# Optimization experiments

Hardware: AMD Instinct MI355X
Metric: run time of the kernel (lower is better)

## Reference

```python
import jax, jax.numpy as jnp
import numpy as np

D, H, DH, FF = 768, 12, 64, 3072

def setup_inputs() -> dict:
    key = jax.random.key(0)
    ks = iter(jax.random.split(key, 40))
    B, Li, Lt = 128, 197, 64
    nrm = lambda shape, s=0.02: (jax.random.normal(next(ks), shape, jnp.float32) * s)
    inp = {}
    inp['image_feats'] = jax.random.normal(next(ks), (B, Li, D), jnp.float32)
    inp['image_att_score'] = jax.random.uniform(next(ks), (B, Li), jnp.float32)
    inp['text_feats'] = jax.random.normal(next(ks), (B, Lt, D), jnp.float32)
    inp['text_att_score'] = jax.random.uniform(next(ks), (B, Lt), jnp.float32)
    inp['tokens'] = jax.random.randint(next(ks), (B, Lt), 0, 1000)
    # BatchNorm1d bottlenecks (inference: running stats)
    for p in ('img', 'txt'):
        inp[f'bn_{p}_g'] = jnp.ones((D,), jnp.float32)
        inp[f'bn_{p}_b'] = jnp.zeros((D,), jnp.float32)
        inp[f'bn_{p}_m'] = nrm((D,), 0.1)
        inp[f'bn_{p}_v'] = jax.random.uniform(next(ks), (D,), jnp.float32, 0.5, 1.5)
    # ResidualAttention (1 layer, cross): ln1, ln2, qkv/out proj, mlp 768->3072->768
    inp['ln1_g'] = jnp.ones((D,), jnp.float32); inp['ln1_b'] = jnp.zeros((D,), jnp.float32)
    inp['ln2_g'] = jnp.ones((D,), jnp.float32); inp['ln2_b'] = jnp.zeros((D,), jnp.float32)
    for n in ('Wq', 'Wk', 'Wv', 'Wo'):
        inp[n] = nrm((D, D))
    for n in ('bq', 'bk', 'bv', 'bo'):
        inp[n] = jnp.zeros((D,), jnp.float32)
    inp['W1'] = nrm((D, FF)); inp['b1'] = jnp.zeros((FF,), jnp.float32)
    inp['W2'] = nrm((FF, D)); inp['b2'] = jnp.zeros((D,), jnp.float32)
    inp['img_K'] = 59   # int(197 * 0.3)
    inp['text_K'] = 19  # int(64 * 0.3)
    return inp

def _ln(x, g, b):
    mu = jnp.mean(x, -1, keepdims=True)
    v = jnp.mean((x - mu) ** 2, -1, keepdims=True)
    return (x - mu) * jax.lax.rsqrt(v + 1e-5) * g + b

def _bn(x, g, b, m, v):
    return (x - m) * jax.lax.rsqrt(v + 1e-5) * g + b

def _cross_block(x, y, key_mask, ln1_g, ln1_b, ln2_g, ln2_b,
                 Wq, bq, Wk, bk, Wv, bv, Wo, bo, W1, b1, W2, b2):
    # cross-attn: queries from x, keys/values from y; pre-LN residual block
    B, Lq, _ = x.shape
    Lk = y.shape[1]
    qn = _ln(x, ln1_g, ln1_b)
    kn = _ln(y, ln1_g, ln1_b)
    q = (qn @ Wq + bq).reshape(B, Lq, H, DH)
    k = (kn @ Wk + bk).reshape(B, Lk, H, DH)
    v = (kn @ Wv + bv).reshape(B, Lk, H, DH)
    scores = jnp.einsum('bqhd,bkhd->bhqk', q, k) / np.float32(np.sqrt(DH))
    if key_mask is not None:  # True = padding -> masked out
        scores = jnp.where(key_mask[:, None, None, :], jnp.float32(-1e9), scores)
    a = jax.nn.softmax(scores, axis=-1)
    att = jnp.einsum('bhqk,bkhd->bqhd', a, v).reshape(B, Lq, D) @ Wo + bo
    x = x + att
    h = _ln(x, ln2_g, ln2_b)
    x = x + jax.nn.gelu(h @ W1 + b1, approximate=False) @ W2 + b2
    return x

def _select(feats, score, K):
    # zero CLS score, full descending sort via top_k, gather token subsets
    L = score.shape[1]
    score = score * jnp.concatenate([jnp.zeros_like(score[:, :1]), jnp.ones_like(score[:, 1:])], axis=1)
    _, idx = jax.lax.top_k(score, L)  # [B, L] sorted desc
    cls = feats[:, :1, :]
    sel1 = jnp.take_along_axis(feats, idx[:, :K, None], axis=1)
    sel2 = jnp.take_along_axis(feats, idx[:, K:2 * K, None], axis=1)
    return jnp.concatenate([cls, sel1], 1), jnp.concatenate([cls, sel2], 1)

def reference(image_feats, image_att_score, text_feats, text_att_score, tokens,
              bn_img_g, bn_img_b, bn_img_m, bn_img_v,
              bn_txt_g, bn_txt_b, bn_txt_m, bn_txt_v,
              ln1_g, ln1_b, ln2_g, ln2_b,
              Wq, bq, Wk, bk, Wv, bv, Wo, bo, W1, b1, W2, b2,
              img_K, text_K):
    blk = lambda x, y, m: _cross_block(x, y, m, ln1_g, ln1_b, ln2_g, ln2_b,
                                       Wq, bq, Wk, bk, Wv, bv, Wo, bo, W1, b1, W2, b2)
    img_global = _bn(image_feats[:, 0, :], bn_img_g, bn_img_b, bn_img_m, bn_img_v)
    text_global = _bn(text_feats[:, 0, :], bn_txt_g, bn_txt_b, bn_txt_m, bn_txt_v)
    text_masks = (tokens == 0)  # True where padding
    img_sel1, img_sel2 = _select(image_feats, image_att_score, img_K)
    image_part1 = blk(img_sel1, image_feats, None)
    image_part2 = blk(img_sel2, image_feats, None)
    txt_sel1, txt_sel2 = _select(text_feats, text_att_score, text_K)
    text_part1 = blk(txt_sel1, text_feats, text_masks)
    text_part2 = blk(txt_sel2, text_feats, text_masks)
    return (img_global, text_global, image_part1, image_part2, text_part1, text_part2)
```

## Files before the change

### kernel.cpp

```cpp
#include <hip/hip_runtime.h>

typedef unsigned short u16;
typedef __bf16 bf16x8 __attribute__((ext_vector_type(8)));
typedef float f32x4 __attribute__((ext_vector_type(4)));

__device__ __forceinline__ float b2f(u16 u) { return __builtin_bit_cast(float, (unsigned)u << 16); }
__device__ __forceinline__ u16 f2b(float f) {
  unsigned x = __builtin_bit_cast(unsigned, f);
  x += 0x7fffu + ((x >> 16) & 1u);
  return (u16)(x >> 16);
}

__device__ __forceinline__ void gload16(const u16* g, u16* l) {
  auto gp = (__attribute__((address_space(1))) void*)(void*)const_cast<u16*>(g);
  auto lp = (__attribute__((address_space(3))) void*)(void*)l;
  __builtin_amdgcn_global_load_lds(gp, lp, 16, 0, 0);
}

__device__ __forceinline__ f32x4 mfma16(bf16x8 a, bf16x8 b, f32x4 c) {
  return __builtin_amdgcn_mfma_f32_16x16x32_bf16(a, b, c, 0, 0, 0);
}

__device__ __forceinline__ float gelu_fast(float v) {
  float u = v * (0.7978845608028654f + 0.03567740813636141f * v * v);
  float e = __expf(2.0f * u);
  float th = 1.0f - 2.0f / (e + 1.0f);
  return 0.5f * v * (1.0f + th);
}

__global__ __launch_bounds__(256) void transpose_k(const float* __restrict__ in, u16* __restrict__ out,
                                                   int R, int C) {
  __shared__ float tile[32][33];
  const int bx = blockIdx.x * 32, by = blockIdx.y * 32;
  const int x = threadIdx.x;
  for (int yy = threadIdx.y; yy < 32; yy += 8) tile[yy][x] = in[(size_t)(by + yy) * C + bx + x];
  __syncthreads();
  for (int yy = threadIdx.y; yy < 32; yy += 8) out[(size_t)(bx + yy) * R + by + x] = f2b(tile[x][yy]);
}

__global__ __launch_bounds__(256) void bn_kernel(const float* __restrict__ feats, int Lrow,
                                                 const float* g, const float* b, const float* m, const float* v,
                                                 float* __restrict__ out) {
  const int bb = blockIdx.x;
  const float* row = feats + (size_t)bb * Lrow * 768;
  for (int d = threadIdx.x; d < 768; d += 256) {
    float x = row[d];
    out[bb * 768 + d] = (x - m[d]) * (1.0f / sqrtf(v[d] + 1e-5f)) * g[d] + b[d];
  }
}

__global__ __launch_bounds__(256) void topk_sel(const float* __restrict__ score, int L, int Ksel,
                                                int* __restrict__ sel, int Lq) {
  __shared__ float s[256];
  const int b = blockIdx.x;
  const int stride2 = 128 * Lq;
  for (int i = threadIdx.x; i < L; i += 256) {
    float v = score[b * L + i];
    s[i] = (i == 0) ? 0.0f : v;
  }
  __syncthreads();
  for (int i = threadIdx.x; i < L; i += 256) {
    float si = s[i];
    int rank = 0;
    for (int j = 0; j < L; ++j) {
      float sj = s[j];
      rank += (sj > si) || (sj == si && j < i);
    }
    if (rank < Ksel) sel[b * Lq + rank + 1] = i;
    else if (rank < 2 * Ksel) sel[stride2 + b * Lq + (rank - Ksel) + 1] = i;
  }
  if (threadIdx.x == 0) { sel[b * Lq] = 0; sel[stride2 + b * Lq] = 0; }
}

__global__ __launch_bounds__(256) void ln_rows(const float* __restrict__ x, const float* g, const float* b,
                                               u16* __restrict__ out) {
  const int row = blockIdx.x * 4 + (threadIdx.x >> 6);
  const int l = threadIdx.x & 63;
  const float* xr = x + (size_t)row * 768;
  float v[12]; float s = 0.f;
#pragma unroll
  for (int i = 0; i < 12; ++i) { v[i] = xr[l + i * 64]; s += v[i]; }
  for (int d = 1; d < 64; d <<= 1) s += __shfl_xor(s, d);
  const float mu = s * (1.0f / 768.0f);
  float q = 0.f;
#pragma unroll
  for (int i = 0; i < 12; ++i) { float t = v[i] - mu; q += t * t; }
  for (int d = 1; d < 64; d <<= 1) q += __shfl_xor(q, d);
  const float rs = 1.0f / sqrtf(q * (1.0f / 768.0f) + 1e-5f);
#pragma unroll
  for (int i = 0; i < 12; ++i) {
    int c = l + i * 64;
    out[(size_t)row * 768 + c] = f2b((v[i] - mu) * rs * g[c] + b[c]);
  }
}

__global__ __launch_bounds__(128) void gather_kernel(const int* __restrict__ sel, const u16* __restrict__ kn,
                                                     const float* __restrict__ feats, u16* __restrict__ qn,
                                                     float* __restrict__ xs, int Lq, int Lsrc) {
  const int q = blockIdx.x, by = blockIdx.y;
  const int p = by >> 7, b = by & 127;
  const int row = (p * 128 + b) * Lq + q;
  const int src = sel[row];
  const uint4* sq = (const uint4*)(kn + ((size_t)b * Lsrc + src) * 768);
  uint4* dq = (uint4*)(qn + (size_t)row * 768);
  for (int c = threadIdx.x; c < 96; c += 128) dq[c] = sq[c];
  const float4* sx = (const float4*)(feats + ((size_t)b * Lsrc + src) * 768);
  float4* dx = (float4*)(xs + (size_t)row * 768);
  for (int c = threadIdx.x; c < 192; c += 128) dx[c] = sx[c];
}

enum { EPI_PLAIN = 0, EPI_QSCALE = 1, EPI_GELU = 2, EPI_RES_FADD = 3, EPI_RES_OUT = 4 };

template <int EPI>
__global__ __launch_bounds__(256) void gemm_bt(const u16* __restrict__ A, const u16* __restrict__ Bt,
                                               const float* __restrict__ bias, const float* __restrict__ res,
                                               void* __restrict__ outp, int M, int N, int K) {
  __shared__ alignas(16) u16 As[128 * 64];
  __shared__ alignas(16) u16 Bs[128 * 64];
  const int tid = threadIdx.x, l = tid & 63, w = tid >> 6;
  const int nwg = gridDim.x * gridDim.y;
  {
  }
  int lin = blockIdx.y * gridDim.x + blockIdx.x;
  const int q8 = nwg >> 3, r8 = nwg & 7;
  const int xcd = lin & 7, pos = lin >> 3;
  const int nl = (xcd < r8) ? (xcd * (q8 + 1) + pos) : (r8 * (q8 + 1) + (xcd - r8) * q8 + pos);
  const int m0 = (nl / gridDim.x) * 128, n0 = (nl % gridDim.x) * 128;
  const int wm = (w & 1) * 64, wn = (w >> 1) * 64;
  f32x4 acc[4][4] = {};
  for (int k0 = 0; k0 < K; k0 += 64) {
#pragma unroll
    for (int p = 0; p < 4; ++p) {
      const int s = p * 256 + tid;
      const int row = s >> 3, ch = (s & 7) ^ (row & 7);
      gload16(A + (size_t)(m0 + row) * K + k0 + ch * 8, &As[s * 8]);
    }
#pragma unroll
    for (int p = 0; p < 4; ++p) {
      const int s = p * 256 + tid;
      const int row = s >> 3, ch = (s & 7) ^ (row & 7);
      gload16(Bt + (size_t)(n0 + row) * K + k0 + ch * 8, &Bs[s * 8]);
    }
    __syncthreads();
#pragma unroll
    for (int kk = 0; kk < 2; ++kk) {
      bf16x8 af[4], bfr[4];
#pragma unroll
      for (int i = 0; i < 4; ++i) {
        const int arow = wm + i * 16 + (l & 15);
        af[i] = *(const bf16x8*)&As[arow * 64 + ((((kk * 4 + (l >> 4))) ^ (arow & 7)) << 3)];
        const int brow = wn + i * 16 + (l & 15);
        bfr[i] = *(const bf16x8*)&Bs[brow * 64 + ((((kk * 4 + (l >> 4))) ^ (brow & 7)) << 3)];
      }
#pragma unroll
      for (int mi = 0; mi < 4; ++mi)
#pragma unroll
        for (int ni = 0; ni < 4; ++ni) acc[mi][ni] = mfma16(af[mi], bfr[ni], acc[mi][ni]);
    }
    __syncthreads();
  }
  const int r4 = (l >> 4) * 4, c16 = l & 15;
#pragma unroll
  for (int mi = 0; mi < 4; ++mi) {
#pragma unroll
    for (int ni = 0; ni < 4; ++ni) {
      const int gn = n0 + wn + ni * 16 + c16;
      const float bia = bias[gn];
#pragma unroll
      for (int j = 0; j < 4; ++j) {
        const int gm = m0 + wm + mi * 16 + r4 + j;
        const size_t off = (size_t)gm * N + gn;
        float v = acc[mi][ni][j] + bia;
        if constexpr (EPI == EPI_QSCALE) {
          ((u16*)outp)[off] = f2b(v * 0.125f);
        } else if constexpr (EPI == EPI_GELU) {
          ((u16*)outp)[off] = f2b(gelu_fast(v));
        } else if constexpr (EPI == EPI_RES_FADD || EPI == EPI_RES_OUT) {
          ((float*)outp)[off] = v + res[off];
        } else {
          ((u16*)outp)[off] = f2b(v);
        }
      }
    }
  }
}

template <int LQP, int LKP, int LQ, int LK, bool MASK>
__global__ __launch_bounds__(256) void attn2(const u16* __restrict__ Q, const u16* __restrict__ Kb,
                                             const u16* __restrict__ Vb, const int* __restrict__ toks,
                                             u16* __restrict__ O) {
  constexpr int LKS = LKP + 8;
  const int h = blockIdx.x, by = blockIdx.y;
  const int p = by & 1, bb = by >> 1;
  const int tid = threadIdx.x, l = tid & 63, w = tid >> 6;
  const size_t qrow0 = (size_t)(p * 128 + bb) * LQ;
  const u16* Qg = Q + qrow0 * 768 + h * 64;
  const u16* Kg = Kb + (size_t)bb * LK * 768 + h * 64;
  const u16* Vg = Vb + (size_t)bb * LK * 768 + h * 64;

  __shared__ alignas(16) u16 Qs[LQP * 64];
  __shared__ alignas(16) u16 KV[64 * LKS];
  __shared__ alignas(16) u16 Ss[LQP * LKS];
  __shared__ int tokLds[MASK ? LKP : 1];

  for (int s = tid; s < LQP * 8; s += 256) {
    int row = s >> 3, d8 = (s & 7) ^ (row & 7);
    int gr = row < LQ ? row : LQ - 1;
    gload16(Qg + (size_t)gr * 768 + d8 * 8, &Qs[s * 8]);
  }
  for (int s = tid; s < LKP * 8; s += 256) {
    int row = s >> 3, d8 = (s & 7) ^ (row & 7);
    int gr = row < LK ? row : LK - 1;
    gload16(Kg + (size_t)gr * 768 + d8 * 8, &KV[s * 8]);
  }
  if (MASK)
    for (int c = tid; c < LKP; c += 256) tokLds[c] = (c < LK) ? toks[bb * LK + c] : 1;
  __syncthreads();

  for (int nt = w; nt < LKP / 16; nt += 4) {
    const int brow = nt * 16 + (l & 15);
#pragma unroll
    for (int mt = 0; mt < LQP / 16; ++mt) {
      const int arow = mt * 16 + (l & 15);
      f32x4 a_ = {0.f, 0.f, 0.f, 0.f};
#pragma unroll
      for (int kk = 0; kk < 2; ++kk) {
        bf16x8 av = *(const bf16x8*)&Qs[arow * 64 + (((kk * 4 + (l >> 4)) ^ (arow & 7)) << 3)];
        bf16x8 bv = *(const bf16x8*)&KV[brow * 64 + (((kk * 4 + (l >> 4)) ^ (brow & 7)) << 3)];
        a_ = mfma16(av, bv, a_);
      }
      const int r0 = mt * 16 + (l >> 4) * 4, cc = nt * 16 + (l & 15);
#pragma unroll
      for (int j = 0; j < 4; ++j) Ss[(r0 + j) * LKS + cc] = f2b(a_[j]);
    }
  }
  __syncthreads();

  {
    const int kcol = tid & 31, d8 = tid >> 5;
#pragma unroll
    for (int kb = 0; kb < LKP / 32; ++kb) {
      const int k = kb * 32 + kcol;
      alignas(16) u16 tmp[8] = {0, 0, 0, 0, 0, 0, 0, 0};
      if (k < LK) *(uint4*)tmp = *(const uint4*)(Vg + (size_t)k * 768 + d8 * 8);
#pragma unroll
      for (int j = 0; j < 8; ++j) KV[(d8 * 8 + j) * LKS + k] = tmp[j];
    }
  }
  constexpr int NCH = (LKP + 63) / 64;
  for (int r = w; r < LQ; r += 4) {
    float sv[NCH];
    float mx = -INFINITY;
#pragma unroll
    for (int i = 0; i < NCH; ++i) {
      int c = l + (i << 6);
      float s = -INFINITY;
      if (c < LK) {
        s = b2f(Ss[r * LKS + c]);
        if (MASK && tokLds[c] == 0) s = -1e9f;
      }
      sv[i] = s;
      mx = fmaxf(mx, s);
    }
    for (int d = 1; d < 64; d <<= 1) mx = fmaxf(mx, __shfl_xor(mx, d));
    float sum = 0.f;
#pragma unroll
    for (int i = 0; i < NCH; ++i) { float e = __expf(sv[i] - mx); sv[i] = e; sum += e; }
    for (int d = 1; d < 64; d <<= 1) sum += __shfl_xor(sum, d);
    const float inv = 1.0f / sum;
#pragma unroll
    for (int i = 0; i < NCH; ++i) {
      int c = l + (i << 6);
      if (c < LKP) Ss[r * LKS + c] = f2b(sv[i] * inv);
    }
  }
  __syncthreads();

  for (int mt = w; mt < LQP / 16; mt += 4) {
    const int arow = mt * 16 + (l & 15);
#pragma unroll
    for (int nt = 0; nt < 4; ++nt) {
      f32x4 a_ = {0.f, 0.f, 0.f, 0.f};
#pragma unroll
      for (int kk = 0; kk < LKP; kk += 32) {
        bf16x8 av = *(const bf16x8*)&Ss[arow * LKS + kk + (l >> 4) * 8];
        bf16x8 bv = *(const bf16x8*)&KV[(nt * 16 + (l & 15)) * LKS + kk + (l >> 4) * 8];
        a_ = mfma16(av, bv, a_);
      }
      const int r0 = mt * 16 + (l >> 4) * 4, c16 = l & 15;
#pragma unroll
      for (int j = 0; j < 4; ++j) {
        int r = r0 + j;
        if (r < LQ) O[(qrow0 + r) * 768 + h * 64 + nt * 16 + c16] = f2b(a_[j]);
      }
    }
  }
}

extern "C" void kernel_launch(void* const* d_in, const int* in_sizes, int n_in,
                              void* d_out, int out_size, void* d_ws, size_t ws_size,
                              hipStream_t stream) {
  (void)in_sizes; (void)n_in; (void)out_size; (void)ws_size;
  const float* image_feats = (const float*)d_in[0];
  const float* image_att = (const float*)d_in[1];
  const float* text_feats = (const float*)d_in[2];
  const float* text_att = (const float*)d_in[3];
  const int* tokens = (const int*)d_in[4];
  const float* bn_img_g = (const float*)d_in[5];
  const float* bn_img_b = (const float*)d_in[6];
  const float* bn_img_m = (const float*)d_in[7];
  const float* bn_img_v = (const float*)d_in[8];
  const float* bn_txt_g = (const float*)d_in[9];
  const float* bn_txt_b = (const float*)d_in[10];
  const float* bn_txt_m = (const float*)d_in[11];
  const float* bn_txt_v = (const float*)d_in[12];
  const float* ln1_g = (const float*)d_in[13];
  const float* ln1_b = (const float*)d_in[14];
  const float* ln2_g = (const float*)d_in[15];
  const float* ln2_b = (const float*)d_in[16];
  const float* Wq = (const float*)d_in[17];
  const float* Wk = (const float*)d_in[18];
  const float* Wv = (const float*)d_in[19];
  const float* Wo = (const float*)d_in[20];
  const float* bq = (const float*)d_in[21];
  const float* bk = (const float*)d_in[22];
  const float* bv = (const float*)d_in[23];
  const float* bo = (const float*)d_in[24];
  const float* W1 = (const float*)d_in[25];
  const float* b1 = (const float*)d_in[26];
  const float* W2 = (const float*)d_in[27];
  const float* b2 = (const float*)d_in[28];

  float* out = (float*)d_out;
  char* wsp = (char*)d_ws;
  size_t off = 0;
  auto alloc = [&](size_t bytes) -> void* {
    void* p = wsp + off;
    off += (bytes + 255) & ~(size_t)255;
    return p;
  };
  u16* WqT = (u16*)alloc(768 * 768 * 2);
  u16* WkT = (u16*)alloc(768 * 768 * 2);
  u16* WvT = (u16*)alloc(768 * 768 * 2);
  u16* WoT = (u16*)alloc(768 * 768 * 2);
  u16* W1T = (u16*)alloc((size_t)768 * 3072 * 2);
  u16* W2T = (u16*)alloc((size_t)768 * 3072 * 2);
  char* kvbase = (char*)(wsp + off);
  u16* kn_i = (u16*)alloc((size_t)25216 * 768 * 2);
  u16* Kb_i = (u16*)alloc((size_t)25216 * 768 * 2);
  u16* Vb_i = (u16*)alloc((size_t)25216 * 768 * 2);
  u16* kn_t = (u16*)alloc((size_t)8192 * 768 * 2);
  u16* Kb_t = (u16*)alloc((size_t)8192 * 768 * 2);
  u16* Vb_t = (u16*)alloc((size_t)8192 * 768 * 2);
  u16* gb = (u16*)kvbase;
  int* sel_i = (int*)alloc(2 * 128 * 60 * 4);
  int* sel_t = (int*)alloc(2 * 128 * 20 * 4);
  u16* qn = (u16*)alloc((size_t)20480 * 768 * 2);
  float* xs = (float*)alloc((size_t)20480 * 768 * 4);
  u16* Qb = (u16*)alloc((size_t)20480 * 768 * 2);

  const dim3 tb(32, 8);
  transpose_k<<<dim3(24, 24), tb, 0, stream>>>(Wq, WqT, 768, 768);
  transpose_k<<<dim3(24, 24), tb, 0, stream>>>(Wk, WkT, 768, 768);
  transpose_k<<<dim3(24, 24), tb, 0, stream>>>(Wv, WvT, 768, 768);
  transpose_k<<<dim3(24, 24), tb, 0, stream>>>(Wo, WoT, 768, 768);
  transpose_k<<<dim3(96, 24), tb, 0, stream>>>(W1, W1T, 768, 3072);
  transpose_k<<<dim3(24, 96), tb, 0, stream>>>(W2, W2T, 3072, 768);

  bn_kernel<<<128, 256, 0, stream>>>(image_feats, 197, bn_img_g, bn_img_b, bn_img_m, bn_img_v, out);
  bn_kernel<<<128, 256, 0, stream>>>(text_feats, 64, bn_txt_g, bn_txt_b, bn_txt_m, bn_txt_v, out + 98304);

  topk_sel<<<128, 256, 0, stream>>>(image_att, 197, 59, sel_i, 60);
  topk_sel<<<128, 256, 0, stream>>>(text_att, 64, 19, sel_t, 20);

  ln_rows<<<25216 / 4, 256, 0, stream>>>(image_feats, ln1_g, ln1_b, kn_i);
  gemm_bt<EPI_PLAIN><<<dim3(6, 197), 256, 0, stream>>>(kn_i, WkT, bk, nullptr, Kb_i, 25216, 768, 768);
  gemm_bt<EPI_PLAIN><<<dim3(6, 197), 256, 0, stream>>>(kn_i, WvT, bv, nullptr, Vb_i, 25216, 768, 768);
  ln_rows<<<8192 / 4, 256, 0, stream>>>(text_feats, ln1_g, ln1_b, kn_t);
  gemm_bt<EPI_PLAIN><<<dim3(6, 64), 256, 0, stream>>>(kn_t, WkT, bk, nullptr, Kb_t, 8192, 768, 768);
  gemm_bt<EPI_PLAIN><<<dim3(6, 64), 256, 0, stream>>>(kn_t, WvT, bv, nullptr, Vb_t, 8192, 768, 768);

  gather_kernel<<<dim3(60, 256), 128, 0, stream>>>(sel_i, kn_i, image_feats, qn, xs, 60, 197);
  gather_kernel<<<dim3(20, 256), 128, 0, stream>>>(sel_t, kn_t, text_feats, qn + (size_t)15360 * 768,
                                                   xs + (size_t)15360 * 768, 20, 64);

  gemm_bt<EPI_QSCALE><<<dim3(6, 160), 256, 0, stream>>>(qn, WqT, bq, nullptr, Qb, 20480, 768, 768);

  attn2<64, 224, 60, 197, false><<<dim3(12, 256), 256, 0, stream>>>(Qb, Kb_i, Vb_i, nullptr, qn);
  attn2<32, 64, 20, 64, true><<<dim3(12, 256), 256, 0, stream>>>(Qb + (size_t)15360 * 768, Kb_t, Vb_t,
                                                                 tokens, qn + (size_t)15360 * 768);

  gemm_bt<EPI_RES_FADD><<<dim3(6, 160), 256, 0, stream>>>(qn, WoT, bo, xs, xs, 20480, 768, 768);
  ln_rows<<<20480 / 4, 256, 0, stream>>>(xs, ln2_g, ln2_b, Qb);
  gemm_bt<EPI_GELU><<<dim3(24, 160), 256, 0, stream>>>(Qb, W1T, b1, nullptr, gb, 20480, 3072, 768);
  gemm_bt<EPI_RES_OUT><<<dim3(6, 160), 256, 0, stream>>>(gb, W2T, b2, xs, out + 196608, 20480, 768, 3072);
}
```

Baseline: 796.1 us.

## Replace GEMM with 256x128-tile triple-buffered pipelined kernel

Replaces the single-buffered 128x128 GEMM with a 256x128 tile kernel that stages K-slices of 32 into a three-deep LDS ring via async global-to-LDS loads, with explicit vmcnt waits and barriers, plus MFMA priority hints. Larger tiles raise arithmetic intensity per block and the ring overlaps memory with compute, removing the load-then-sync stalls of the old loop. Image K/V buffers are padded to 25344 rows so the 256-row tiles fit; the extra rows read and write past the real 25216-row data into padding, and the larger register footprint risks lower occupancy.

Result: slower. 817.9 us (+2.7%).

```diff
diff --git a/kernel.cpp b/kernel.cpp
--- a/kernel.cpp
+++ b/kernel.cpp
@@ -112,77 +112,122 @@
 enum { EPI_PLAIN = 0, EPI_QSCALE = 1, EPI_GELU = 2, EPI_RES_FADD = 3, EPI_RES_OUT = 4 };
 
 template <int EPI>
-__global__ __launch_bounds__(256) void gemm_bt(const u16* __restrict__ A, const u16* __restrict__ Bt,
-                                               const float* __restrict__ bias, const float* __restrict__ res,
-                                               void* __restrict__ outp, int M, int N, int K) {
-  __shared__ alignas(16) u16 As[128 * 64];
-  __shared__ alignas(16) u16 Bs[128 * 64];
+__device__ __forceinline__ void epi_write(float v, size_t off, void* outp, const float* res) {
+  if constexpr (EPI == EPI_QSCALE) {
+    ((u16*)outp)[off] = f2b(v * 0.125f);
+  } else if constexpr (EPI == EPI_GELU) {
+    ((u16*)outp)[off] = f2b(gelu_fast(v));
+  } else if constexpr (EPI == EPI_RES_FADD || EPI == EPI_RES_OUT) {
+    ((float*)outp)[off] = v + res[off];
+  } else {
+    ((u16*)outp)[off] = f2b(v);
+  }
+}
+
+template <int EPI>
+__global__ __launch_bounds__(256, 2) void gemm_v4(const u16* __restrict__ A, const u16* __restrict__ Bt,
+                                                  const float* __restrict__ bias, const float* __restrict__ res,
+                                                  void* __restrict__ outp, int M, int N, int K) {
+  __shared__ alignas(16) u16 As[3 * 128 * 64];
+  __shared__ alignas(16) u16 Bs[3 * 64 * 64];
   const int tid = threadIdx.x, l = tid & 63, w = tid >> 6;
   const int nwg = gridDim.x * gridDim.y;
-  {
-  }
   int lin = blockIdx.y * gridDim.x + blockIdx.x;
   const int q8 = nwg >> 3, r8 = nwg & 7;
   const int xcd = lin & 7, pos = lin >> 3;
   const int nl = (xcd < r8) ? (xcd * (q8 + 1) + pos) : (r8 * (q8 + 1) + (xcd - r8) * q8 + pos);
-  const int m0 = (nl / gridDim.x) * 128, n0 = (nl % gridDim.x) * 128;
-  const int wm = (w & 1) * 64, wn = (w >> 1) * 64;
-  f32x4 acc[4][4] = {};
-  for (int k0 = 0; k0 < K; k0 += 64) {
+  const int m0 = (nl / gridDim.x) * 256, n0 = (nl % gridDim.x) * 128;
+  const int wr = w & 1, wc = w >> 1;
+  f32x4 acc[8][4] = {};
+
+  const u16* apt[4];
+  int adst[4];
+  const u16* bpt[2];
+  int bdst[2];
+#pragma unroll
+  for (int p = 0; p < 4; ++p) {
+    const int s = p * 256 + tid;
+    const int lrow = s >> 3, v = (s & 7) ^ (lrow & 7);
+    apt[p] = A + (size_t)(m0 + (v >> 2) * 128 + lrow) * K + (v & 3) * 8;
+    adst[p] = s * 8;
+  }
+#pragma unroll
+  for (int p = 0; p < 2; ++p) {
+    const int s = p * 256 + tid;
+    const int lrow = s >> 3, v = (s & 7) ^ (lrow & 7);
+    bpt[p] = Bt + (size_t)(n0 + (v >> 2) * 64 + lrow) * K + (v & 3) * 8;
+    bdst[p] = s * 8;
+  }
+  auto STAGE = [&](int buf) {
 #pragma unroll
     for (int p = 0; p < 4; ++p) {
-      const int s = p * 256 + tid;
-      const int row = s >> 3, ch = (s & 7) ^ (row & 7);
-      gload16(A + (size_t)(m0 + row) * K + k0 + ch * 8, &As[s * 8]);
-    }
-#pragma unroll
-    for (int p = 0; p < 4; ++p) {
-      const int s = p * 256 + tid;
-      const int row = s >> 3, ch = (s & 7) ^ (row & 7);
-      gload16(Bt + (size_t)(n0 + row) * K + k0 + ch * 8, &Bs[s * 8]);
-    }
-    __syncthreads();
-#pragma unroll
-    for (int kk = 0; kk < 2; ++kk) {
-      bf16x8 af[4], bfr[4];
-#pragma unroll
-      for (int i = 0; i < 4; ++i) {
-        const int arow = wm + i * 16 + (l & 15);
-        af[i] = *(const bf16x8*)&As[arow * 64 + ((((kk * 4 + (l >> 4))) ^ (arow & 7)) << 3)];
-        const int brow = wn + i * 16 + (l & 15);
-        bfr[i] = *(const bf16x8*)&Bs[brow * 64 + ((((kk * 4 + (l >> 4))) ^ (brow & 7)) << 3)];
+      gload16(apt[p], &As[buf * 8192 + adst[p]]);
+      apt[p] += 32;
+    }
+#pragma unroll
+    for (int p = 0; p < 2; ++p) {
+      gload16(bpt[p], &Bs[buf * 4096 + bdst[p]]);
+      bpt[p] += 32;
+    }
+  };
+
+  auto COMPUTE = [&](int buf) {
+    bf16x8 bfr[4], af[8];
+#pragma unroll
+    for (int j = 0; j < 4; ++j) {
+      const int fr = j * 16 + (l & 15);
+      const int slot = ((l >> 4) | (wc << 2)) ^ (fr & 7);
+      bfr[j] = *(const bf16x8*)&Bs[buf * 4096 + fr * 64 + slot * 8];
+    }
+#pragma unroll
+    for (int i = 0; i < 8; ++i) {
+      const int fr = i * 16 + (l & 15);
+      const int slot = ((l >> 4) | (wr << 2)) ^ (fr & 7);
+      af[i] = *(const bf16x8*)&As[buf * 8192 + fr * 64 + slot * 8];
+    }
+    __builtin_amdgcn_s_setprio(1);
+#pragma unroll
+    for (int i = 0; i < 8; ++i)
+#pragma unroll
+      for (int j = 0; j < 4; ++j) acc[i][j] = mfma16(af[i], bfr[j], acc[i][j]);
+    __builtin_amdgcn_s_setprio(0);
+  };
+
+  const int NT = K >> 5;
+  STAGE(0);
+  STAGE(1);
+  int b0 = 0, b2 = 2;
+  for (int t = 0; t < NT; ++t) {
+    if (t + 2 < NT) {
+      STAGE(b2);
+      asm volatile("s_waitcnt vmcnt(12)" ::: "memory");
+    } else if (t + 2 == NT) {
+      asm volatile("s_waitcnt vmcnt(6)" ::: "memory");
+    } else {
+      asm volatile("s_waitcnt vmcnt(0)" ::: "memory");
+    }
+    __builtin_amdgcn_sched_barrier(0);
+    __builtin_amdgcn_s_barrier();
+    __builtin_amdgcn_sched_barrier(0);
+    COMPUTE(b0);
+    __builtin_amdgcn_s_barrier();
+    b0 = (b0 == 2) ? 0 : b0 + 1;
+    b2 = (b2 == 2) ? 0 : b2 + 1;
+  }
+
+  const int r4 = (l >> 4) * 4, c16 = l & 15;
+#pragma unroll
+  for (int i = 0; i < 8; ++i)
+#pragma unroll
+    for (int j = 0; j < 4; ++j) {
+      const int gn = n0 + wc * 64 + j * 16 + c16;
+      const float bia = bias[gn];
+#pragma unroll
+      for (int jj = 0; jj < 4; ++jj) {
+        const int gm = m0 + wr * 128 + i * 16 + r4 + jj;
+        epi_write<EPI>(acc[i][j][jj] + bia, (size_t)gm * N + gn, outp, res);
       }
-#pragma unroll
-      for (int mi = 0; mi < 4; ++mi)
-#pragma unroll
-        for (int ni = 0; ni < 4; ++ni) acc[mi][ni] = mfma16(af[mi], bfr[ni], acc[mi][ni]);
-    }
-    __syncthreads();
-  }
-  const int r4 = (l >> 4) * 4, c16 = l & 15;
-#pragma unroll
-  for (int mi = 0; mi < 4; ++mi) {
-#pragma unroll
-    for (int ni = 0; ni < 4; ++ni) {
-      const int gn = n0 + wn + ni * 16 + c16;
-      const float bia = bias[gn];
-#pragma unroll
-      for (int j = 0; j < 4; ++j) {
-        const int gm = m0 + wm + mi * 16 + r4 + j;
-        const size_t off = (size_t)gm * N + gn;
-        float v = acc[mi][ni][j] + bia;
-        if constexpr (EPI == EPI_QSCALE) {
-          ((u16*)outp)[off] = f2b(v * 0.125f);
-        } else if constexpr (EPI == EPI_GELU) {
-          ((u16*)outp)[off] = f2b(gelu_fast(v));
-        } else if constexpr (EPI == EPI_RES_FADD || EPI == EPI_RES_OUT) {
-          ((float*)outp)[off] = v + res[off];
-        } else {
-          ((u16*)outp)[off] = f2b(v);
-        }
-      }
-    }
-  }
+    }
 }
 
 template <int LQP, int LKP, int LQ, int LK, bool MASK>
@@ -346,9 +391,9 @@
   u16* W1T = (u16*)alloc((size_t)768 * 3072 * 2);
   u16* W2T = (u16*)alloc((size_t)768 * 3072 * 2);
   char* kvbase = (char*)(wsp + off);
-  u16* kn_i = (u16*)alloc((size_t)25216 * 768 * 2);
-  u16* Kb_i = (u16*)alloc((size_t)25216 * 768 * 2);
-  u16* Vb_i = (u16*)alloc((size_t)25216 * 768 * 2);
+  u16* kn_i = (u16*)alloc((size_t)25344 * 768 * 2);
+  u16* Kb_i = (u16*)alloc((size_t)25344 * 768 * 2);
+  u16* Vb_i = (u16*)alloc((size_t)25344 * 768 * 2);
   u16* kn_t = (u16*)alloc((size_t)8192 * 768 * 2);
   u16* Kb_t = (u16*)alloc((size_t)8192 * 768 * 2);
   u16* Vb_t = (u16*)alloc((size_t)8192 * 768 * 2);
@@ -374,24 +419,24 @@
   topk_sel<<<128, 256, 0, stream>>>(text_att, 64, 19, sel_t, 20);
 
   ln_rows<<<25216 / 4, 256, 0, stream>>>(image_feats, ln1_g, ln1_b, kn_i);
-  gemm_bt<EPI_PLAIN><<<dim3(6, 197), 256, 0, stream>>>(kn_i, WkT, bk, nullptr, Kb_i, 25216, 768, 768);
-  gemm_bt<EPI_PLAIN><<<dim3(6, 197), 256, 0, stream>>>(kn_i, WvT, bv, nullptr, Vb_i, 25216, 768, 768);
+  gemm_v4<EPI_PLAIN><<<dim3(6, 99), 256, 0, stream>>>(kn_i, WkT, bk, nullptr, Kb_i, 25344, 768, 768);
+  gemm_v4<EPI_PLAIN><<<dim3(6, 99), 256, 0, stream>>>(kn_i, WvT, bv, nullptr, Vb_i, 25344, 768, 768);
   ln_rows<<<8192 / 4, 256, 0, stream>>>(text_feats, ln1_g, ln1_b, kn_t);
-  gemm_bt<EPI_PLAIN><<<dim3(6, 64), 256, 0, stream>>>(kn_t, WkT, bk, nullptr, Kb_t, 8192, 768, 768);
-  gemm_bt<EPI_PLAIN><<<dim3(6, 64), 256, 0, stream>>>(kn_t, WvT, bv, nullptr, Vb_t, 8192, 768, 768);
+  gemm_v4<EPI_PLAIN><<<dim3(6, 32), 256, 0, stream>>>(kn_t, WkT, bk, nullptr, Kb_t, 8192, 768, 768);
+  gemm_v4<EPI_PLAIN><<<dim3(6, 32), 256, 0, stream>>>(kn_t, WvT, bv, nullptr, Vb_t, 8192, 768, 768);
 
   gather_kernel<<<dim3(60, 256), 128, 0, stream>>>(sel_i, kn_i, image_feats, qn, xs, 60, 197);
   gather_kernel<<<dim3(20, 256), 128, 0, stream>>>(sel_t, kn_t, text_feats, qn + (size_t)15360 * 768,
                                                    xs + (size_t)15360 * 768, 20, 64);
 
-  gemm_bt<EPI_QSCALE><<<dim3(6, 160), 256, 0, stream>>>(qn, WqT, bq, nullptr, Qb, 20480, 768, 768);
+  gemm_v4<EPI_QSCALE><<<dim3(6, 80), 256, 0, stream>>>(qn, WqT, bq, nullptr, Qb, 20480, 768, 768);
 
   attn2<64, 224, 60, 197, false><<<dim3(12, 256), 256, 0, stream>>>(Qb, Kb_i, Vb_i, nullptr, qn);
   attn2<32, 64, 20, 64, true><<<dim3(12, 256), 256, 0, stream>>>(Qb + (size_t)15360 * 768, Kb_t, Vb_t,
                                                                  tokens, qn + (size_t)15360 * 768);
 
-  gemm_bt<EPI_RES_FADD><<<dim3(6, 160), 256, 0, stream>>>(qn, WoT, bo, xs, xs, 20480, 768, 768);
+  gemm_v4<EPI_RES_FADD><<<dim3(6, 80), 256, 0, stream>>>(qn, WoT, bo, xs, xs, 20480, 768, 768);
   ln_rows<<<20480 / 4, 256, 0, stream>>>(xs, ln2_g, ln2_b, Qb);
-  gemm_bt<EPI_GELU><<<dim3(24, 160), 256, 0, stream>>>(Qb, W1T, b1, nullptr, gb, 20480, 3072, 768);
-  gemm_bt<EPI_RES_OUT><<<dim3(6, 160), 256, 0, stream>>>(gb, W2T, b2, xs, out + 196608, 20480, 768, 3072);
-}
+  gemm_v4<EPI_GELU><<<dim3(24, 80), 256, 0, stream>>>(Qb, W1T, b1, nullptr, gb, 20480, 3072, 768);
+  gemm_v4<EPI_RES_OUT><<<dim3(6, 80), 256, 0, stream>>>(gb, W2T, b2, xs, out + 196608, 20480, 768, 3072);
+}
```
